# Kernel optimization log

Measured on AMD Instinct MI355X. Metric: run time of the kernel, lower is better.

The kernel has to match this reference:

```python
import jax, jax.numpy as jnp
import numpy as np

HIDDEN = 256
HEADS = 8
HEAD_DIM = HIDDEN // HEADS
N = 4096
EPS = 1e-5


def setup_inputs() -> dict:
    key = jax.random.key(0)
    ks = jax.random.split(key, 16)
    s = HIDDEN ** -0.5
    inp = {
        "A": jax.random.uniform(ks[0], (N, N), dtype=jnp.float32),
        "h": jax.random.normal(ks[1], (N, HIDDEN), dtype=jnp.float32),
        # Linear layers stored torch-style as [out, in]
        "Wq": jax.random.normal(ks[2], (HIDDEN, HIDDEN), jnp.float32) * s,
        "bq": jnp.zeros((HIDDEN,), jnp.float32),
        "Wk": jax.random.normal(ks[3], (HIDDEN, HIDDEN), jnp.float32) * s,
        "bk": jnp.zeros((HIDDEN,), jnp.float32),
        "Wv": jax.random.normal(ks[4], (HIDDEN, HIDDEN), jnp.float32) * s,
        "bv": jnp.zeros((HIDDEN,), jnp.float32),
        "Wo": jax.random.normal(ks[5], (HIDDEN, HIDDEN), jnp.float32) * s,
        "bo": jnp.zeros((HIDDEN,), jnp.float32),
        "W1": jax.random.normal(ks[6], (2 * HIDDEN, HIDDEN), jnp.float32) * s,
        "c1": jnp.zeros((2 * HIDDEN,), jnp.float32),
        "W2": jax.random.normal(ks[7], (HIDDEN, 2 * HIDDEN), jnp.float32) * (2 * HIDDEN) ** -0.5,
        "c2": jnp.zeros((HIDDEN,), jnp.float32),
        "g1": jnp.ones((HIDDEN,), jnp.float32),
        "be1": jnp.zeros((HIDDEN,), jnp.float32),
        "g2": jnp.ones((HIDDEN,), jnp.float32),
        "be2": jnp.zeros((HIDDEN,), jnp.float32),
    }
    return inp


def _batchnorm(x, gamma, beta):
    # BatchNorm1d training mode: biased batch stats over node axis
    mean = x.mean(axis=0)
    var = ((x - mean) ** 2).mean(axis=0)
    return (x - mean) * jax.lax.rsqrt(var + EPS) * gamma + beta


def _mha(A, h, Wq, bq, Wk, bk, Wv, bv, Wo, bo):
    n = h.shape[0]
    scaling = HEAD_DIM ** -0.5
    # NOTE: raw reshape [N, H*d] -> (H, N, d), exactly as the torch code (no transpose)
    q = ((h @ Wq.T + bq).reshape(HEADS, n, HEAD_DIM)) * scaling
    k = (h @ Wk.T + bk).reshape(HEADS, n, HEAD_DIM)
    v = (h @ Wv.T + bv).reshape(HEADS, n, HEAD_DIM)
    t = jnp.einsum('hnd,hmd->hnm', q, k)          # [H, N, N]
    attn = jax.nn.softmax(t * A, axis=2)          # multiplicative adjacency mask
    out = jnp.einsum('hnm,hmd->hnd', attn, v)     # [H, N, d]
    return out.reshape(n, -1) @ Wo.T + bo         # raw reshape back, as in torch


def reference(A, h, Wq, bq, Wk, bk, Wv, bv, Wo, bo, W1, c1, W2, c2, g1, be1, g2, be2):
    h1 = h
    x = _mha(A, h, Wq, bq, Wk, bk, Wv, bv, Wo, bo)
    x = _batchnorm(x + h1, g1, be1)
    h2 = x
    x = jax.nn.relu(x @ W1.T + c1) @ W2.T + c2
    return _batchnorm(h2 + x, g2, be2)
```

## Files before the change

kernel.cpp:

```cpp
#include <hip/hip_runtime.h>

#define N_NODES 4096
#define HID 256
#define NHEADS 8
#define HDIM 32
#define EPSV 1e-5f
#define M2LOG 11.541560327111707f

typedef __bf16 bf16x8 __attribute__((ext_vector_type(8)));
typedef __bf16 bf16x4 __attribute__((ext_vector_type(4)));
typedef float f32x4 __attribute__((ext_vector_type(4)));

__device__ inline float fexp2(float x) {
    float r;
    asm("v_exp_f32 %0, %1" : "=v"(r) : "v"(x));
    return r;
}

__device__ inline uint4 pack8(float4 a, float4 b) {
    bf16x8 p;
    p[0]=(__bf16)a.x; p[1]=(__bf16)a.y; p[2]=(__bf16)a.z; p[3]=(__bf16)a.w;
    p[4]=(__bf16)b.x; p[5]=(__bf16)b.y; p[6]=(__bf16)b.z; p[7]=(__bf16)b.w;
    return __builtin_bit_cast(uint4, p);
}
__device__ inline float4 nmad4(float4 x, float4 s, float4 sh) {
    return make_float4(fmaf(x.x,s.x,sh.x), fmaf(x.y,s.y,sh.y),
                       fmaf(x.z,s.z,sh.z), fmaf(x.w,s.w,sh.w));
}

__launch_bounds__(256)
__global__ void gemm_mfma(const float* __restrict__ X, const float* __restrict__ W,
                          const float* __restrict__ bias, const float* __restrict__ resid,
                          float* __restrict__ C,
                          const float* __restrict__ nscale, const float* __restrict__ nshift,
                          const float* __restrict__ rscale, const float* __restrict__ rshift,
                          int M, int N, int K, float scale, int do_relu) {
    __shared__ uint4 xl[2][512];
    __shared__ uint4 wl[2][512];
    const int bm = blockIdx.x * 64, bn = blockIdx.y * 64;
    const int t = threadIdx.x;
    const int w = t >> 6, l = t & 63, g = l >> 4, nl = l & 15;
    const int srow = t >> 3, seg = t & 7;
    const int sx = (seg & 3) << 1;
    const int d0 = seg*64 + (srow ^ sx);
    const int d1 = seg*64 + ((srow + 32) ^ sx);
    const float* xp = X + (size_t)(bm + srow)*K + seg*8;
    const float* wp = W + (size_t)(bn + srow)*K + seg*8;
    const size_t rstep = (size_t)32*K;

    f32x4 acc[4];
    #pragma unroll
    for (int nf = 0; nf < 4; ++nf) acc[nf] = (f32x4){0.f,0.f,0.f,0.f};

    {
        float4 x0 = *(const float4*)(xp),          x1 = *(const float4*)(xp + 4);
        float4 x2 = *(const float4*)(xp + rstep),  x3 = *(const float4*)(xp + rstep + 4);
        if (nscale) {
            float4 s0 = *(const float4*)(nscale + seg*8), s1 = *(const float4*)(nscale + seg*8 + 4);
            float4 h0 = *(const float4*)(nshift + seg*8), h1 = *(const float4*)(nshift + seg*8 + 4);
            x0 = nmad4(x0,s0,h0); x1 = nmad4(x1,s1,h1);
            x2 = nmad4(x2,s0,h0); x3 = nmad4(x3,s1,h1);
        }
        float4 w0 = *(const float4*)(wp),          w1 = *(const float4*)(wp + 4);
        float4 w2 = *(const float4*)(wp + rstep),  w3 = *(const float4*)(wp + rstep + 4);
        xl[0][d0] = pack8(x0, x1); xl[0][d1] = pack8(x2, x3);
        wl[0][d0] = pack8(w0, w1); wl[0][d1] = pack8(w2, w3);
    }
    __syncthreads();

    for (int k0 = 0; k0 < K; k0 += 64) {
        const int cur = (k0 >> 6) & 1;
        const bool nxt = (k0 + 64) < K;
        float4 nx0, nx1, nx2, nx3, nw0, nw1, nw2, nw3;
        if (nxt) {
            const int kk = k0 + 64;
            nx0 = *(const float4*)(xp + kk);          nx1 = *(const float4*)(xp + kk + 4);
            nx2 = *(const float4*)(xp + rstep + kk);  nx3 = *(const float4*)(xp + rstep + kk + 4);
            if (nscale) {
                float4 s0 = *(const float4*)(nscale + kk + seg*8), s1 = *(const float4*)(nscale + kk + seg*8 + 4);
                float4 h0 = *(const float4*)(nshift + kk + seg*8), h1 = *(const float4*)(nshift + kk + seg*8 + 4);
                nx0 = nmad4(nx0,s0,h0); nx1 = nmad4(nx1,s1,h1);
                nx2 = nmad4(nx2,s0,h0); nx3 = nmad4(nx3,s1,h1);
            }
            nw0 = *(const float4*)(wp + kk);          nw1 = *(const float4*)(wp + kk + 4);
            nw2 = *(const float4*)(wp + rstep + kk);  nw3 = *(const float4*)(wp + rstep + kk + 4);
        }
        __builtin_amdgcn_s_setprio(1);
        #pragma unroll
        for (int ks = 0; ks < 2; ++ks) {
            bf16x8 af = __builtin_bit_cast(bf16x8, xl[cur][(ks*4 + g)*64 + ((w*16 + nl) ^ (g << 1))]);
            #pragma unroll
            for (int nf = 0; nf < 4; ++nf) {
                bf16x8 bfr = __builtin_bit_cast(bf16x8, wl[cur][(ks*4 + g)*64 + ((nf*16 + nl) ^ (g << 1))]);
                acc[nf] = __builtin_amdgcn_mfma_f32_16x16x32_bf16(af, bfr, acc[nf], 0, 0, 0);
            }
        }
        __builtin_amdgcn_s_setprio(0);
        if (nxt) {
            xl[cur^1][d0] = pack8(nx0, nx1); xl[cur^1][d1] = pack8(nx2, nx3);
            wl[cur^1][d0] = pack8(nw0, nw1); wl[cur^1][d1] = pack8(nw2, nw3);
        }
        __syncthreads();
    }

    #pragma unroll
    for (int nf = 0; nf < 4; ++nf) {
        const int col = bn + nf*16 + nl;
        const float bb = bias[col];
        float rs = 1.f, rh = 0.f;
        if (rscale) { rs = rscale[col]; rh = rshift[col]; }
        #pragma unroll
        for (int r = 0; r < 4; ++r) {
            const int row = bm + w*16 + g*4 + r;
            float v = acc[nf][r] + bb;
            if (resid) {
                float rv = resid[(size_t)row*N + col];
                v += rscale ? fmaf(rv, rs, rh) : rv;
            }
            v *= scale;
            if (do_relu) v = fmaxf(v, 0.f);
            C[(size_t)row*N + col] = v;
        }
    }
}

__launch_bounds__(256)
__global__ void gemm_qkv(const float* __restrict__ X,
                         const float* __restrict__ Wq, const float* __restrict__ Wk,
                         const float* __restrict__ Wv, const float* __restrict__ bq,
                         const float* __restrict__ bk, const float* __restrict__ bv,
                         __bf16* __restrict__ qhat, __bf16* __restrict__ khat,
                         __bf16* __restrict__ vhat) {
    const int K = 256;
    __shared__ uint4 xl[2][512];
    __shared__ uint4 wl[2][512];
    const int z = blockIdx.z;
    const float* W = (z == 0) ? Wq : (z == 1) ? Wk : Wv;
    const float* bias = (z == 0) ? bq : (z == 1) ? bk : bv;
    __bf16* hat = (z == 0) ? qhat : (z == 1) ? khat : vhat;
    const float scale = (z == 0) ? 0.25506595325f : 1.f;

    const int bm = blockIdx.x * 64, bn = blockIdx.y * 64;
    const int t = threadIdx.x;
    const int w = t >> 6, l = t & 63, g = l >> 4, nl = l & 15;
    const int srow = t >> 3, seg = t & 7;
    const int sx = (seg & 3) << 1;
    const int d0 = seg*64 + (srow ^ sx);
    const int d1 = seg*64 + ((srow + 32) ^ sx);
    const float* xp = X + (size_t)(bm + srow)*K + seg*8;
    const float* wp = W + (size_t)(bn + srow)*K + seg*8;
    const size_t rstep = (size_t)32*K;

    f32x4 acc[4];
    #pragma unroll
    for (int nf = 0; nf < 4; ++nf) acc[nf] = (f32x4){0.f,0.f,0.f,0.f};

    {
        float4 x0 = *(const float4*)(xp),          x1 = *(const float4*)(xp + 4);
        float4 x2 = *(const float4*)(xp + rstep),  x3 = *(const float4*)(xp + rstep + 4);
        float4 w0 = *(const float4*)(wp),          w1 = *(const float4*)(wp + 4);
        float4 w2 = *(const float4*)(wp + rstep),  w3 = *(const float4*)(wp + rstep + 4);
        xl[0][d0] = pack8(x0, x1); xl[0][d1] = pack8(x2, x3);
        wl[0][d0] = pack8(w0, w1); wl[0][d1] = pack8(w2, w3);
    }
    __syncthreads();

    for (int k0 = 0; k0 < K; k0 += 64) {
        const int cur = (k0 >> 6) & 1;
        const bool nxt = (k0 + 64) < K;
        float4 nx0, nx1, nx2, nx3, nw0, nw1, nw2, nw3;
        if (nxt) {
            nx0 = *(const float4*)(xp + k0 + 64);          nx1 = *(const float4*)(xp + k0 + 68);
            nx2 = *(const float4*)(xp + rstep + k0 + 64);  nx3 = *(const float4*)(xp + rstep + k0 + 68);
            nw0 = *(const float4*)(wp + k0 + 64);          nw1 = *(const float4*)(wp + k0 + 68);
            nw2 = *(const float4*)(wp + rstep + k0 + 64);  nw3 = *(const float4*)(wp + rstep + k0 + 68);
        }
        __builtin_amdgcn_s_setprio(1);
        #pragma unroll
        for (int ks = 0; ks < 2; ++ks) {
            bf16x8 af = __builtin_bit_cast(bf16x8, xl[cur][(ks*4 + g)*64 + ((w*16 + nl) ^ (g << 1))]);
            #pragma unroll
            for (int nf = 0; nf < 4; ++nf) {
                bf16x8 bfr = __builtin_bit_cast(bf16x8, wl[cur][(ks*4 + g)*64 + ((nf*16 + nl) ^ (g << 1))]);
                acc[nf] = __builtin_amdgcn_mfma_f32_16x16x32_bf16(af, bfr, acc[nf], 0, 0, 0);
            }
        }
        __builtin_amdgcn_s_setprio(0);
        if (nxt) {
            xl[cur^1][d0] = pack8(nx0, nx1); xl[cur^1][d1] = pack8(nx2, nx3);
            wl[cur^1][d0] = pack8(nw0, nw1); wl[cur^1][d1] = pack8(nw2, nw3);
        }
        __syncthreads();
    }

    #pragma unroll
    for (int nf = 0; nf < 4; ++nf) {
        const int col = bn + nf*16 + nl;
        const float bb = bias[col];
        #pragma unroll
        for (int r = 0; r < 4; ++r) {
            const int row = bm + w*16 + g*4 + r;
            float v = (acc[nf][r] + bb) * scale;
            const int hh = row >> 9;
            const int nn = ((row & 511) << 3) | (col >> 5);
            hat[((size_t)(hh*4096 + nn))*32 + (col & 31)] = (__bf16)v;
        }
    }
}

__launch_bounds__(256)
__global__ void transpose_vhat(const __bf16* __restrict__ vhat, __bf16* __restrict__ vT) {
    const int h = blockIdx.y, n0 = blockIdx.x * 64;
    __shared__ __bf16 tile[64][40];
    const int t = threadIdx.x;
    {
        int n = t >> 2, dd0 = (t & 3) * 8;
        *(uint4*)&tile[n][dd0] = *(const uint4*)(vhat + ((size_t)(h*4096 + n0 + n))*32 + dd0);
    }
    __syncthreads();
    {
        int d = t >> 3, ns = (t & 7) * 8;
        uint4 ov;
        __bf16* op = (__bf16*)&ov;
        #pragma unroll
        for (int j = 0; j < 8; ++j) op[j] = tile[ns + j][d];
        *(uint4*)(vT + ((size_t)(h*32 + d))*4096 + n0 + ns) = ov;
    }
}

__launch_bounds__(256)
__global__ void attn_mfma(const __bf16* __restrict__ qh, const __bf16* __restrict__ kh,
                          const __bf16* __restrict__ vT, const float* __restrict__ A,
                          float* __restrict__ Opart, float* __restrict__ Lpart, int mlen) {
    const int h = blockIdx.y;
    const int n0 = blockIdx.x * 64;
    const int z = blockIdx.z;
    const int m_begin = z * mlen, m_end = m_begin + mlen;
    const int t = threadIdx.x;
    const int w = t >> 6, l = t & 63;
    const int g = l >> 4, nl = l & 15;
    const int nlx = nl ^ (g << 1);
    const int nq = n0 + w*16 + nl;

    __shared__ uint4 k_lds[2][256];
    __shared__ uint4 v_lds[2][256];
    __shared__ uint4 p_lds[4][128];

    bf16x8 qf = *(const bf16x8*)(qh + ((size_t)(h*4096 + nq))*32 + g*8);

    f32x4 oacc[2];
    oacc[0] = (f32x4){0.f,0.f,0.f,0.f};
    oacc[1] = (f32x4){0.f,0.f,0.f,0.f};
    float Li = 0.f;
    const float* Arow = A + (size_t)nq * N_NODES;

    const int km_row = t >> 2, km_dseg = t & 3;
    const __bf16* kbase = kh + ((size_t)h*4096 + km_row)*32 + km_dseg*8;
    const int kdst = (((km_row >> 4)*4 + km_dseg) << 4) | ((km_row & 15) ^ (km_dseg << 1));
    const int vd = t >> 3, vmseg = t & 7;
    const __bf16* vbase = vT + ((size_t)h*32 + vd)*4096 + vmseg*8;
    const int vdst = ((((vd >> 4)*2 + (vmseg >> 2))*4 + (vmseg & 3)) << 4) | ((vd & 15) ^ ((vmseg & 3) << 1));

    {
        k_lds[0][kdst] = *(const uint4*)(kbase + (size_t)m_begin*32);
        v_lds[0][vdst] = *(const uint4*)(vbase + m_begin);
    }
    float4 ar0 = *(const float4*)(Arow + m_begin + 0*16 + g*4);
    float4 ar1 = *(const float4*)(Arow + m_begin + 1*16 + g*4);
    float4 ar2 = *(const float4*)(Arow + m_begin + 2*16 + g*4);
    float4 ar3 = *(const float4*)(Arow + m_begin + 3*16 + g*4);
    __syncthreads();

    for (int m0 = m_begin; m0 < m_end; m0 += 64) {
        const int cur = ((m0 - m_begin) >> 6) & 1;
        const bool nxt = (m0 + 64) < m_end;
        uint4 krN, vrN;
        float4 an0, an1, an2, an3;
        if (nxt) {
            krN = *(const uint4*)(kbase + (size_t)(m0 + 64)*32);
            vrN = *(const uint4*)(vbase + (m0 + 64));
            an0 = *(const float4*)(Arow + m0 + 64 + 0*16 + g*4);
            an1 = *(const float4*)(Arow + m0 + 64 + 1*16 + g*4);
            an2 = *(const float4*)(Arow + m0 + 64 + 2*16 + g*4);
            an3 = *(const float4*)(Arow + m0 + 64 + 3*16 + g*4);
        }

        f32x4 st[4];
        __builtin_amdgcn_s_setprio(1);
        #pragma unroll
        for (int tt = 0; tt < 4; ++tt) {
            bf16x8 kf = __builtin_bit_cast(bf16x8, k_lds[cur][(tt*4 + g)*16 + nlx]);
            f32x4 zz = (f32x4){0.f,0.f,0.f,0.f};
            st[tt] = __builtin_amdgcn_mfma_f32_16x16x32_bf16(kf, qf, zz, 0, 0, 0);
        }
        __builtin_amdgcn_s_setprio(0);

        float p[4][4];
        p[0][0]=fexp2(fmaf(st[0][0],ar0.x,-M2LOG)); p[0][1]=fexp2(fmaf(st[0][1],ar0.y,-M2LOG));
        p[0][2]=fexp2(fmaf(st[0][2],ar0.z,-M2LOG)); p[0][3]=fexp2(fmaf(st[0][3],ar0.w,-M2LOG));
        p[1][0]=fexp2(fmaf(st[1][0],ar1.x,-M2LOG)); p[1][1]=fexp2(fmaf(st[1][1],ar1.y,-M2LOG));
        p[1][2]=fexp2(fmaf(st[1][2],ar1.z,-M2LOG)); p[1][3]=fexp2(fmaf(st[1][3],ar1.w,-M2LOG));
        p[2][0]=fexp2(fmaf(st[2][0],ar2.x,-M2LOG)); p[2][1]=fexp2(fmaf(st[2][1],ar2.y,-M2LOG));
        p[2][2]=fexp2(fmaf(st[2][2],ar2.z,-M2LOG)); p[2][3]=fexp2(fmaf(st[2][3],ar2.w,-M2LOG));
        p[3][0]=fexp2(fmaf(st[3][0],ar3.x,-M2LOG)); p[3][1]=fexp2(fmaf(st[3][1],ar3.y,-M2LOG));
        p[3][2]=fexp2(fmaf(st[3][2],ar3.z,-M2LOG)); p[3][3]=fexp2(fmaf(st[3][3],ar3.w,-M2LOG));

        float sm[4];
        #pragma unroll
        for (int tt = 0; tt < 4; ++tt)
            sm[tt] = (p[tt][0] + p[tt][1]) + (p[tt][2] + p[tt][3]);
        Li += (sm[0] + sm[1]) + (sm[2] + sm[3]);

        #pragma unroll
        for (int tt = 0; tt < 4; ++tt) {
            bf16x4 pk;
            #pragma unroll
            for (int r = 0; r < 4; ++r) pk[r] = (__bf16)p[tt][r];
            const int seg = (tt >> 1)*4 + 2*(tt & 1) + (g >> 1);
            const int uw = seg*16 + (nl ^ ((seg & 3) << 1));
            *(bf16x4*)((char*)&p_lds[w][0] + uw*16 + (g & 1)*8) = pk;
        }

        __builtin_amdgcn_s_setprio(1);
        #pragma unroll
        for (int kt = 0; kt < 2; ++kt) {
            bf16x8 pf = __builtin_bit_cast(bf16x8, p_lds[w][(kt*4 + g)*16 + nlx]);
            #pragma unroll
            for (int dt = 0; dt < 2; ++dt) {
                bf16x8 vf = __builtin_bit_cast(bf16x8, v_lds[cur][((dt*2 + kt)*4 + g)*16 + nlx]);
                oacc[dt] = __builtin_amdgcn_mfma_f32_16x16x32_bf16(vf, pf, oacc[dt], 0, 0, 0);
            }
        }
        __builtin_amdgcn_s_setprio(0);

        if (nxt) {
            k_lds[cur^1][kdst] = krN;
            v_lds[cur^1][vdst] = vrN;
            ar0 = an0; ar1 = an1; ar2 = an2; ar3 = an3;
        }
        __syncthreads();
    }

    float* ob = Opart + (((size_t)(z*NHEADS + h))*4096 + nq)*32;
    *(float4*)(ob + 0*16 + g*4) = make_float4(oacc[0][0], oacc[0][1], oacc[0][2], oacc[0][3]);
    *(float4*)(ob + 1*16 + g*4) = make_float4(oacc[1][0], oacc[1][1], oacc[1][2], oacc[1][3]);
    Li += __shfl_xor(Li, 16);
    Li += __shfl_xor(Li, 32);
    if (g == 0) Lpart[(z*NHEADS + h)*4096 + nq] = Li;
}

__launch_bounds__(256)
__global__ void attn_combine(const float* __restrict__ Opart, const float* __restrict__ Lpart,
                             float* __restrict__ AO, int nsplit) {
    const int idx4 = (blockIdx.x * 256 + threadIdx.x) * 4;
    const int hn = idx4 >> 5;
    float L = 0.f;
    float4 acc = make_float4(0.f, 0.f, 0.f, 0.f);
    for (int zz = 0; zz < nsplit; ++zz) {
        L += Lpart[zz*32768 + hn];
        float4 o = *(const float4*)(Opart + (size_t)zz*1048576 + idx4);
        acc.x += o.x; acc.y += o.y; acc.z += o.z; acc.w += o.w;
    }
    const float inv = 1.f / L;
    *(float4*)(AO + idx4) = make_float4(acc.x*inv, acc.y*inv, acc.z*inv, acc.w*inv);
}

__launch_bounds__(256)
__global__ void colstats_part(const float* __restrict__ X, float* __restrict__ ps,
                              float* __restrict__ pq) {
    const int b = blockIdx.x, t = threadIdx.x;
    float s = 0.f, q = 0.f;
    const float* p = X + (size_t)b*64*HID + t;
    #pragma unroll 8
    for (int r = 0; r < 64; ++r) {
        float v = p[r*HID];
        s += v; q = fmaf(v, v, q);
    }
    ps[b*HID + t] = s;
    pq[b*HID + t] = q;
}

__launch_bounds__(256)
__global__ void colstats_fin(const float* __restrict__ ps, const float* __restrict__ pq,
                             const float* __restrict__ gam, const float* __restrict__ bet,
                             float* __restrict__ scl, float* __restrict__ shf) {
    const int c = threadIdx.x;
    float s = 0.f, q = 0.f;
    #pragma unroll 8
    for (int b = 0; b < 64; ++b) { s += ps[b*HID + c]; q += pq[b*HID + c]; }
    const float m = s * (1.f/4096.f);
    const float rstd = rsqrtf(q*(1.f/4096.f) - m*m + EPSV);
    const float sc = rstd * gam[c];
    scl[c] = sc;
    shf[c] = fmaf(-m, sc, bet[c]);
}

__launch_bounds__(256)
__global__ void bnorm_apply4(const float* __restrict__ X, const float* __restrict__ scl,
                             const float* __restrict__ shf, float* __restrict__ Y) {
    const int base = (blockIdx.x * 256 + threadIdx.x) * 4;
    const int c = base & (HID - 1);
    float4 x = *(const float4*)(X + base);
    float4 o;
    o.x = fmaf(x.x, scl[c+0], shf[c+0]);
    o.y = fmaf(x.y, scl[c+1], shf[c+1]);
    o.z = fmaf(x.z, scl[c+2], shf[c+2]);
    o.w = fmaf(x.w, scl[c+3], shf[c+3]);
    *(float4*)(Y + base) = o;
}

extern "C" void kernel_launch(void* const* d_in, const int* in_sizes, int n_in,
                              void* d_out, int out_size, void* d_ws, size_t ws_size,
                              hipStream_t stream) {
    const float* A  = (const float*)d_in[0];
    const float* h  = (const float*)d_in[1];
    const float* Wq = (const float*)d_in[2];
    const float* bq = (const float*)d_in[3];
    const float* Wk = (const float*)d_in[4];
    const float* bk = (const float*)d_in[5];
    const float* Wv = (const float*)d_in[6];
    const float* bv = (const float*)d_in[7];
    const float* Wo = (const float*)d_in[8];
    const float* bo = (const float*)d_in[9];
    const float* W1 = (const float*)d_in[10];
    const float* c1 = (const float*)d_in[11];
    const float* W2 = (const float*)d_in[12];
    const float* c2 = (const float*)d_in[13];
    const float* g1 = (const float*)d_in[14];
    const float* be1= (const float*)d_in[15];
    const float* g2 = (const float*)d_in[16];
    const float* be2= (const float*)d_in[17];

    char* wsb = (char*)d_ws;
    const size_t MiB = (size_t)1 << 20;
    const int nsplit = (ws_size >= 27*MiB) ? 4 : (ws_size >= 19*MiB) ? 2 : 1;
    const int mlen = N_NODES / nsplit;

    __bf16* qhat = (__bf16*)(wsb + 0*MiB);
    __bf16* khat = (__bf16*)(wsb + 2*MiB);
    __bf16* vhat = (__bf16*)(wsb + 4*MiB);
    __bf16* vT   = (__bf16*)(wsb + 6*MiB);
    float* Opart = (float*)(wsb + 8*MiB);
    float* Lpart = (float*)(wsb + 8*MiB + (size_t)nsplit*4*MiB);
    char* statb  = wsb + 8*MiB + (size_t)nsplit*4*MiB + 1*MiB;
    float* partS = (float*)statb;
    float* partQ = partS + 64*HID;
    float* scale1 = partQ + 64*HID;
    float* shift1 = scale1 + HID;
    float* scale2 = shift1 + HID;
    float* shift2 = scale2 + HID;
    float* AO = (float*)(wsb + 0*MiB);
    float* Y1 = (float*)(wsb + 4*MiB);
    float* F1 = (float*)(wsb + 8*MiB);
    float* Y2 = (float*)(wsb + 0*MiB);

    gemm_qkv<<<dim3(64, 4, 3), 256, 0, stream>>>(h, Wq, Wk, Wv, bq, bk, bv, qhat, khat, vhat);
    transpose_vhat<<<dim3(64, 8), 256, 0, stream>>>(vhat, vT);

    attn_mfma<<<dim3(64, 8, nsplit), 256, 0, stream>>>(qhat, khat, vT, A, Opart, Lpart, mlen);
    attn_combine<<<1024, 256, 0, stream>>>(Opart, Lpart, AO, nsplit);

    gemm_mfma<<<dim3(64, 4), 256, 0, stream>>>(AO, Wo, bo, h, Y1,
                                               nullptr, nullptr, nullptr, nullptr,
                                               4096, 256, 256, 1.f, 0);

    colstats_part<<<64, 256, 0, stream>>>(Y1, partS, partQ);
    colstats_fin<<<1, 256, 0, stream>>>(partS, partQ, g1, be1, scale1, shift1);

    gemm_mfma<<<dim3(64, 8), 256, 0, stream>>>(Y1, W1, c1, nullptr, F1,
                                               scale1, shift1, nullptr, nullptr,
                                               4096, 512, 256, 1.f, 1);
    gemm_mfma<<<dim3(64, 4), 256, 0, stream>>>(F1, W2, c2, Y1, Y2,
                                               nullptr, nullptr, scale1, shift1,
                                               4096, 256, 512, 1.f, 0);

    colstats_part<<<64, 256, 0, stream>>>(Y2, partS, partQ);
    colstats_fin<<<1, 256, 0, stream>>>(partS, partQ, g2, be2, scale2, shift2);
    bnorm_apply4<<<1024, 256, 0, stream>>>(Y2, scale2, shift2, (float*)d_out);
}
```

Baseline: 149.5 us.

## Share A tile across all heads per block and store partial outputs in bf16

The attention kernel now runs one 512-thread block per 64-row query tile with one wave per head. The block stages the fp32 adjacency tile in LDS once and shares it across all 8 heads, where before each head re-read A from global memory. K and V fragments are now read straight from global memory instead of being staged in LDS, and each wave handles four 16-row query subtiles. Partial outputs are stored in bf16 and the split count over the key axis doubles. This trades more register pressure, bf16 rounding of partial sums and uncached K/V reads for an eightfold cut in A traffic.

```diff
diff --git a/kernel.cpp b/kernel.cpp
--- a/kernel.cpp
+++ b/kernel.cpp
@@ -228,129 +228,128 @@
     }
 }
 
-__launch_bounds__(256)
+__launch_bounds__(512, 4)
 __global__ void attn_mfma(const __bf16* __restrict__ qh, const __bf16* __restrict__ kh,
                           const __bf16* __restrict__ vT, const float* __restrict__ A,
-                          float* __restrict__ Opart, float* __restrict__ Lpart, int mlen) {
-    const int h = blockIdx.y;
+                          __bf16* __restrict__ Opart, float* __restrict__ Lpart, int mlen) {
+    __shared__ float A_lds[2][64][68];
+    __shared__ __bf16 p_lds[NHEADS][64][40];
+
+    const int t = threadIdx.x;
+    const int w = t >> 6;
+    const int l = t & 63, g = l >> 4, nl = l & 15;
     const int n0 = blockIdx.x * 64;
-    const int z = blockIdx.z;
-    const int m_begin = z * mlen, m_end = m_begin + mlen;
-    const int t = threadIdx.x;
-    const int w = t >> 6, l = t & 63;
-    const int g = l >> 4, nl = l & 15;
-    const int nlx = nl ^ (g << 1);
-    const int nq = n0 + w*16 + nl;
-
-    __shared__ uint4 k_lds[2][256];
-    __shared__ uint4 v_lds[2][256];
-    __shared__ uint4 p_lds[4][128];
-
-    bf16x8 qf = *(const bf16x8*)(qh + ((size_t)(h*4096 + nq))*32 + g*8);
-
-    f32x4 oacc[2];
-    oacc[0] = (f32x4){0.f,0.f,0.f,0.f};
-    oacc[1] = (f32x4){0.f,0.f,0.f,0.f};
-    float Li = 0.f;
-    const float* Arow = A + (size_t)nq * N_NODES;
-
-    const int km_row = t >> 2, km_dseg = t & 3;
-    const __bf16* kbase = kh + ((size_t)h*4096 + km_row)*32 + km_dseg*8;
-    const int kdst = (((km_row >> 4)*4 + km_dseg) << 4) | ((km_row & 15) ^ (km_dseg << 1));
-    const int vd = t >> 3, vmseg = t & 7;
-    const __bf16* vbase = vT + ((size_t)h*32 + vd)*4096 + vmseg*8;
-    const int vdst = ((((vd >> 4)*2 + (vmseg >> 2))*4 + (vmseg & 3)) << 4) | ((vd & 15) ^ ((vmseg & 3) << 1));
-
+    const int z = blockIdx.y;
+    const int m_begin = z * mlen;
+    const int nsteps = mlen >> 6;
+
+    bf16x8 qf[4];
+    #pragma unroll
+    for (int nt = 0; nt < 4; ++nt)
+        qf[nt] = *(const bf16x8*)(qh + ((size_t)(w*4096 + n0 + nt*16 + nl))*32 + g*8);
+
+    f32x4 oacc[4][2];
+    #pragma unroll
+    for (int nt = 0; nt < 4; ++nt) {
+        oacc[nt][0] = (f32x4){0.f,0.f,0.f,0.f};
+        oacc[nt][1] = (f32x4){0.f,0.f,0.f,0.f};
+    }
+    float Li[4] = {0.f, 0.f, 0.f, 0.f};
+
+    const int aq = t >> 3, am = (t & 7) * 8;
+    const float* Abase = A + (size_t)(n0 + aq)*N_NODES + m_begin + am;
     {
-        k_lds[0][kdst] = *(const uint4*)(kbase + (size_t)m_begin*32);
-        v_lds[0][vdst] = *(const uint4*)(vbase + m_begin);
-    }
-    float4 ar0 = *(const float4*)(Arow + m_begin + 0*16 + g*4);
-    float4 ar1 = *(const float4*)(Arow + m_begin + 1*16 + g*4);
-    float4 ar2 = *(const float4*)(Arow + m_begin + 2*16 + g*4);
-    float4 ar3 = *(const float4*)(Arow + m_begin + 3*16 + g*4);
+        float4 a0 = *(const float4*)(Abase);
+        float4 a1 = *(const float4*)(Abase + 4);
+        *(float4*)&A_lds[0][aq][am] = a0;
+        *(float4*)&A_lds[0][aq][am+4] = a1;
+    }
     __syncthreads();
 
-    for (int m0 = m_begin; m0 < m_end; m0 += 64) {
-        const int cur = ((m0 - m_begin) >> 6) & 1;
-        const bool nxt = (m0 + 64) < m_end;
-        uint4 krN, vrN;
-        float4 an0, an1, an2, an3;
-        if (nxt) {
-            krN = *(const uint4*)(kbase + (size_t)(m0 + 64)*32);
-            vrN = *(const uint4*)(vbase + (m0 + 64));
-            an0 = *(const float4*)(Arow + m0 + 64 + 0*16 + g*4);
-            an1 = *(const float4*)(Arow + m0 + 64 + 1*16 + g*4);
-            an2 = *(const float4*)(Arow + m0 + 64 + 2*16 + g*4);
-            an3 = *(const float4*)(Arow + m0 + 64 + 3*16 + g*4);
-        }
-
-        f32x4 st[4];
-        __builtin_amdgcn_s_setprio(1);
-        #pragma unroll
-        for (int tt = 0; tt < 4; ++tt) {
-            bf16x8 kf = __builtin_bit_cast(bf16x8, k_lds[cur][(tt*4 + g)*16 + nlx]);
-            f32x4 zz = (f32x4){0.f,0.f,0.f,0.f};
-            st[tt] = __builtin_amdgcn_mfma_f32_16x16x32_bf16(kf, qf, zz, 0, 0, 0);
-        }
-        __builtin_amdgcn_s_setprio(0);
-
-        float p[4][4];
-        p[0][0]=fexp2(fmaf(st[0][0],ar0.x,-M2LOG)); p[0][1]=fexp2(fmaf(st[0][1],ar0.y,-M2LOG));
-        p[0][2]=fexp2(fmaf(st[0][2],ar0.z,-M2LOG)); p[0][3]=fexp2(fmaf(st[0][3],ar0.w,-M2LOG));
-        p[1][0]=fexp2(fmaf(st[1][0],ar1.x,-M2LOG)); p[1][1]=fexp2(fmaf(st[1][1],ar1.y,-M2LOG));
-        p[1][2]=fexp2(fmaf(st[1][2],ar1.z,-M2LOG)); p[1][3]=fexp2(fmaf(st[1][3],ar1.w,-M2LOG));
-        p[2][0]=fexp2(fmaf(st[2][0],ar2.x,-M2LOG)); p[2][1]=fexp2(fmaf(st[2][1],ar2.y,-M2LOG));
-        p[2][2]=fexp2(fmaf(st[2][2],ar2.z,-M2LOG)); p[2][3]=fexp2(fmaf(st[2][3],ar2.w,-M2LOG));
-        p[3][0]=fexp2(fmaf(st[3][0],ar3.x,-M2LOG)); p[3][1]=fexp2(fmaf(st[3][1],ar3.y,-M2LOG));
-        p[3][2]=fexp2(fmaf(st[3][2],ar3.z,-M2LOG)); p[3][3]=fexp2(fmaf(st[3][3],ar3.w,-M2LOG));
-
-        float sm[4];
-        #pragma unroll
-        for (int tt = 0; tt < 4; ++tt)
-            sm[tt] = (p[tt][0] + p[tt][1]) + (p[tt][2] + p[tt][3]);
-        Li += (sm[0] + sm[1]) + (sm[2] + sm[3]);
-
-        #pragma unroll
-        for (int tt = 0; tt < 4; ++tt) {
-            bf16x4 pk;
+    const __bf16* kbase = kh + (size_t)w*4096*32;
+    const __bf16* vbase = vT + (size_t)w*32*4096;
+
+    for (int s = 0; s < nsteps; ++s) {
+        const int m0 = m_begin + s*64;
+        const int cur = s & 1;
+        const bool nxt = (s + 1) < nsteps;
+        float4 a0n, a1n;
+        if (nxt) {
+            a0n = *(const float4*)(Abase + (s+1)*64);
+            a1n = *(const float4*)(Abase + (s+1)*64 + 4);
+        }
+
+        #pragma unroll
+        for (int half = 0; half < 2; ++half) {
+            bf16x8 vf[2];
             #pragma unroll
-            for (int r = 0; r < 4; ++r) pk[r] = (__bf16)p[tt][r];
-            const int seg = (tt >> 1)*4 + 2*(tt & 1) + (g >> 1);
-            const int uw = seg*16 + (nl ^ ((seg & 3) << 1));
-            *(bf16x4*)((char*)&p_lds[w][0] + uw*16 + (g & 1)*8) = pk;
-        }
-
-        __builtin_amdgcn_s_setprio(1);
-        #pragma unroll
-        for (int kt = 0; kt < 2; ++kt) {
-            bf16x8 pf = __builtin_bit_cast(bf16x8, p_lds[w][(kt*4 + g)*16 + nlx]);
+            for (int dt = 0; dt < 2; ++dt)
+                vf[dt] = *(const bf16x8*)(vbase + (size_t)(dt*16 + nl)*4096 + m0 + half*32 + g*8);
+
             #pragma unroll
-            for (int dt = 0; dt < 2; ++dt) {
-                bf16x8 vf = __builtin_bit_cast(bf16x8, v_lds[cur][((dt*2 + kt)*4 + g)*16 + nlx]);
-                oacc[dt] = __builtin_amdgcn_mfma_f32_16x16x32_bf16(vf, pf, oacc[dt], 0, 0, 0);
-            }
-        }
-        __builtin_amdgcn_s_setprio(0);
-
-        if (nxt) {
-            k_lds[cur^1][kdst] = krN;
-            v_lds[cur^1][vdst] = vrN;
-            ar0 = an0; ar1 = an1; ar2 = an2; ar3 = an3;
+            for (int ts = 0; ts < 2; ++ts) {
+                const int tt = half*2 + ts;
+                bf16x8 kf = *(const bf16x8*)(kbase + (size_t)(m0 + tt*16 + nl)*32 + g*8);
+                f32x4 st[4];
+                __builtin_amdgcn_s_setprio(1);
+                #pragma unroll
+                for (int nt = 0; nt < 4; ++nt) {
+                    f32x4 zz = (f32x4){0.f,0.f,0.f,0.f};
+                    st[nt] = __builtin_amdgcn_mfma_f32_16x16x32_bf16(kf, qf[nt], zz, 0, 0, 0);
+                }
+                __builtin_amdgcn_s_setprio(0);
+                #pragma unroll
+                for (int nt = 0; nt < 4; ++nt) {
+                    const f32x4 a4 = *(const f32x4*)&A_lds[cur][nt*16 + nl][tt*16 + g*4];
+                    float p0 = fexp2(fmaf(st[nt][0], a4[0], -M2LOG));
+                    float p1 = fexp2(fmaf(st[nt][1], a4[1], -M2LOG));
+                    float p2 = fexp2(fmaf(st[nt][2], a4[2], -M2LOG));
+                    float p3 = fexp2(fmaf(st[nt][3], a4[3], -M2LOG));
+                    Li[nt] += (p0 + p1) + (p2 + p3);
+                    bf16x4 pk;
+                    pk[0] = (__bf16)p0; pk[1] = (__bf16)p1;
+                    pk[2] = (__bf16)p2; pk[3] = (__bf16)p3;
+                    *(bf16x4*)&p_lds[w][nt*16 + nl][ts*16 + g*4] = pk;
+                }
+            }
+
+            __builtin_amdgcn_s_setprio(1);
+            #pragma unroll
+            for (int nt = 0; nt < 4; ++nt) {
+                bf16x8 pf = *(const bf16x8*)&p_lds[w][nt*16 + nl][g*8];
+                #pragma unroll
+                for (int dt = 0; dt < 2; ++dt)
+                    oacc[nt][dt] = __builtin_amdgcn_mfma_f32_16x16x32_bf16(vf[dt], pf, oacc[nt][dt], 0, 0, 0);
+            }
+            __builtin_amdgcn_s_setprio(0);
+        }
+
+        if (nxt) {
+            *(float4*)&A_lds[cur^1][aq][am]   = a0n;
+            *(float4*)&A_lds[cur^1][aq][am+4] = a1n;
         }
         __syncthreads();
     }
 
-    float* ob = Opart + (((size_t)(z*NHEADS + h))*4096 + nq)*32;
-    *(float4*)(ob + 0*16 + g*4) = make_float4(oacc[0][0], oacc[0][1], oacc[0][2], oacc[0][3]);
-    *(float4*)(ob + 1*16 + g*4) = make_float4(oacc[1][0], oacc[1][1], oacc[1][2], oacc[1][3]);
-    Li += __shfl_xor(Li, 16);
-    Li += __shfl_xor(Li, 32);
-    if (g == 0) Lpart[(z*NHEADS + h)*4096 + nq] = Li;
-}
-
-__launch_bounds__(256)
-__global__ void attn_combine(const float* __restrict__ Opart, const float* __restrict__ Lpart,
+    #pragma unroll
+    for (int nt = 0; nt < 4; ++nt) {
+        Li[nt] += __shfl_xor(Li[nt], 16);
+        Li[nt] += __shfl_xor(Li[nt], 32);
+        const size_t obase = ((size_t)((z*NHEADS + w)*4096) + n0 + nt*16 + nl)*32;
+        #pragma unroll
+        for (int dt = 0; dt < 2; ++dt) {
+            bf16x4 ok;
+            ok[0] = (__bf16)oacc[nt][dt][0]; ok[1] = (__bf16)oacc[nt][dt][1];
+            ok[2] = (__bf16)oacc[nt][dt][2]; ok[3] = (__bf16)oacc[nt][dt][3];
+            *(bf16x4*)(Opart + obase + dt*16 + g*4) = ok;
+        }
+        if (g == 0)
+            Lpart[(z*NHEADS + w)*4096 + n0 + nt*16 + nl] = Li[nt];
+    }
+}
+
+__launch_bounds__(256)
+__global__ void attn_combine(const __bf16* __restrict__ Opart, const float* __restrict__ Lpart,
                              float* __restrict__ AO, int nsplit) {
     const int idx4 = (blockIdx.x * 256 + threadIdx.x) * 4;
     const int hn = idx4 >> 5;
@@ -358,8 +357,9 @@
     float4 acc = make_float4(0.f, 0.f, 0.f, 0.f);
     for (int zz = 0; zz < nsplit; ++zz) {
         L += Lpart[zz*32768 + hn];
-        float4 o = *(const float4*)(Opart + (size_t)zz*1048576 + idx4);
-        acc.x += o.x; acc.y += o.y; acc.z += o.z; acc.w += o.w;
+        bf16x4 o = *(const bf16x4*)(Opart + (size_t)zz*1048576 + idx4);
+        acc.x += (float)o[0]; acc.y += (float)o[1];
+        acc.z += (float)o[2]; acc.w += (float)o[3];
     }
     const float inv = 1.f / L;
     *(float4*)(AO + idx4) = make_float4(acc.x*inv, acc.y*inv, acc.z*inv, acc.w*inv);
@@ -433,16 +433,16 @@
 
     char* wsb = (char*)d_ws;
     const size_t MiB = (size_t)1 << 20;
-    const int nsplit = (ws_size >= 27*MiB) ? 4 : (ws_size >= 19*MiB) ? 2 : 1;
+    const int nsplit = (ws_size >= 26*MiB) ? 8 : (ws_size >= 18*MiB) ? 4 : 2;
     const int mlen = N_NODES / nsplit;
 
     __bf16* qhat = (__bf16*)(wsb + 0*MiB);
     __bf16* khat = (__bf16*)(wsb + 2*MiB);
     __bf16* vhat = (__bf16*)(wsb + 4*MiB);
     __bf16* vT   = (__bf16*)(wsb + 6*MiB);
-    float* Opart = (float*)(wsb + 8*MiB);
-    float* Lpart = (float*)(wsb + 8*MiB + (size_t)nsplit*4*MiB);
-    char* statb  = wsb + 8*MiB + (size_t)nsplit*4*MiB + 1*MiB;
+    __bf16* Opart = (__bf16*)(wsb + 8*MiB);
+    float* Lpart = (float*)(wsb + 8*MiB + (size_t)nsplit*2*MiB);
+    char* statb  = wsb + 8*MiB + (size_t)nsplit*2*MiB + 1*MiB;
     float* partS = (float*)statb;
     float* partQ = partS + 64*HID;
     float* scale1 = partQ + 64*HID;
@@ -457,7 +457,7 @@
     gemm_qkv<<<dim3(64, 4, 3), 256, 0, stream>>>(h, Wq, Wk, Wv, bq, bk, bv, qhat, khat, vhat);
     transpose_vhat<<<dim3(64, 8), 256, 0, stream>>>(vhat, vT);
 
-    attn_mfma<<<dim3(64, 8, nsplit), 256, 0, stream>>>(qhat, khat, vT, A, Opart, Lpart, mlen);
+    attn_mfma<<<dim3(64, nsplit), 512, 0, stream>>>(qhat, khat, vT, A, Opart, Lpart, mlen);
     attn_combine<<<1024, 256, 0, stream>>>(Opart, Lpart, AO, nsplit);
 
     gemm_mfma<<<dim3(64, 4), 256, 0, stream>>>(AO, Wo, bo, h, Y1,
```

New measurement: 166.8 us. 11.5% more time.

## Load K/V fragments straight from global memory and raise split count

Applied to the files above, without the earlier changes.

The attention kernel stops staging K and V tiles in double-buffered shared memory behind block-wide barriers. Each wave now loads its MFMA operand fragments directly from global memory, handles the 64-column step in two 32-column halves with a smaller per-wave P buffer, and never calls __syncthreads. The split-K factor over the key dimension also goes up (up to 8, depending on workspace size), which adds blocks but also more partial output traffic for the combine kernel. The cost is redundant global and L2 reads of K/V across the four waves, and loads that are no longer prefetched a step ahead.

```diff
diff --git a/kernel.cpp b/kernel.cpp
--- a/kernel.cpp
+++ b/kernel.cpp
@@ -232,19 +232,17 @@
 __global__ void attn_mfma(const __bf16* __restrict__ qh, const __bf16* __restrict__ kh,
                           const __bf16* __restrict__ vT, const float* __restrict__ A,
                           float* __restrict__ Opart, float* __restrict__ Lpart, int mlen) {
-    const int h = blockIdx.y;
-    const int n0 = blockIdx.x * 64;
-    const int z = blockIdx.z;
-    const int m_begin = z * mlen, m_end = m_begin + mlen;
+    __shared__ uint4 p_lds[4][64];
     const int t = threadIdx.x;
     const int w = t >> 6, l = t & 63;
     const int g = l >> 4, nl = l & 15;
     const int nlx = nl ^ (g << 1);
+    const int h = blockIdx.y;
+    const int n0 = blockIdx.x * 64;
+    const int z = blockIdx.z;
+    const int m_begin = z * mlen;
+    const int nsteps = mlen >> 6;
     const int nq = n0 + w*16 + nl;
-
-    __shared__ uint4 k_lds[2][256];
-    __shared__ uint4 v_lds[2][256];
-    __shared__ uint4 p_lds[4][128];
 
     bf16x8 qf = *(const bf16x8*)(qh + ((size_t)(h*4096 + nq))*32 + g*8);
 
@@ -252,101 +250,77 @@
     oacc[0] = (f32x4){0.f,0.f,0.f,0.f};
     oacc[1] = (f32x4){0.f,0.f,0.f,0.f};
     float Li = 0.f;
-    const float* Arow = A + (size_t)nq * N_NODES;
-
-    const int km_row = t >> 2, km_dseg = t & 3;
-    const __bf16* kbase = kh + ((size_t)h*4096 + km_row)*32 + km_dseg*8;
-    const int kdst = (((km_row >> 4)*4 + km_dseg) << 4) | ((km_row & 15) ^ (km_dseg << 1));
-    const int vd = t >> 3, vmseg = t & 7;
-    const __bf16* vbase = vT + ((size_t)h*32 + vd)*4096 + vmseg*8;
-    const int vdst = ((((vd >> 4)*2 + (vmseg >> 2))*4 + (vmseg & 3)) << 4) | ((vd & 15) ^ ((vmseg & 3) << 1));
-
-    {
-        k_lds[0][kdst] = *(const uint4*)(kbase + (size_t)m_begin*32);
-        v_lds[0][vdst] = *(const uint4*)(vbase + m_begin);
-    }
-    float4 ar0 = *(const float4*)(Arow + m_begin + 0*16 + g*4);
-    float4 ar1 = *(const float4*)(Arow + m_begin + 1*16 + g*4);
-    float4 ar2 = *(const float4*)(Arow + m_begin + 2*16 + g*4);
-    float4 ar3 = *(const float4*)(Arow + m_begin + 3*16 + g*4);
-    __syncthreads();
-
-    for (int m0 = m_begin; m0 < m_end; m0 += 64) {
-        const int cur = ((m0 - m_begin) >> 6) & 1;
-        const bool nxt = (m0 + 64) < m_end;
-        uint4 krN, vrN;
-        float4 an0, an1, an2, an3;
-        if (nxt) {
-            krN = *(const uint4*)(kbase + (size_t)(m0 + 64)*32);
-            vrN = *(const uint4*)(vbase + (m0 + 64));
-            an0 = *(const float4*)(Arow + m0 + 64 + 0*16 + g*4);
-            an1 = *(const float4*)(Arow + m0 + 64 + 1*16 + g*4);
-            an2 = *(const float4*)(Arow + m0 + 64 + 2*16 + g*4);
-            an3 = *(const float4*)(Arow + m0 + 64 + 3*16 + g*4);
-        }
-
-        f32x4 st[4];
-        __builtin_amdgcn_s_setprio(1);
-        #pragma unroll
-        for (int tt = 0; tt < 4; ++tt) {
-            bf16x8 kf = __builtin_bit_cast(bf16x8, k_lds[cur][(tt*4 + g)*16 + nlx]);
-            f32x4 zz = (f32x4){0.f,0.f,0.f,0.f};
-            st[tt] = __builtin_amdgcn_mfma_f32_16x16x32_bf16(kf, qf, zz, 0, 0, 0);
-        }
-        __builtin_amdgcn_s_setprio(0);
-
-        float p[4][4];
-        p[0][0]=fexp2(fmaf(st[0][0],ar0.x,-M2LOG)); p[0][1]=fexp2(fmaf(st[0][1],ar0.y,-M2LOG));
-        p[0][2]=fexp2(fmaf(st[0][2],ar0.z,-M2LOG)); p[0][3]=fexp2(fmaf(st[0][3],ar0.w,-M2LOG));
-        p[1][0]=fexp2(fmaf(st[1][0],ar1.x,-M2LOG)); p[1][1]=fexp2(fmaf(st[1][1],ar1.y,-M2LOG));
-        p[1][2]=fexp2(fmaf(st[1][2],ar1.z,-M2LOG)); p[1][3]=fexp2(fmaf(st[1][3],ar1.w,-M2LOG));
-        p[2][0]=fexp2(fmaf(st[2][0],ar2.x,-M2LOG)); p[2][1]=fexp2(fmaf(st[2][1],ar2.y,-M2LOG));
-        p[2][2]=fexp2(fmaf(st[2][2],ar2.z,-M2LOG)); p[2][3]=fexp2(fmaf(st[2][3],ar2.w,-M2LOG));
-        p[3][0]=fexp2(fmaf(st[3][0],ar3.x,-M2LOG)); p[3][1]=fexp2(fmaf(st[3][1],ar3.y,-M2LOG));
-        p[3][2]=fexp2(fmaf(st[3][2],ar3.z,-M2LOG)); p[3][3]=fexp2(fmaf(st[3][3],ar3.w,-M2LOG));
-
-        float sm[4];
-        #pragma unroll
-        for (int tt = 0; tt < 4; ++tt)
-            sm[tt] = (p[tt][0] + p[tt][1]) + (p[tt][2] + p[tt][3]);
-        Li += (sm[0] + sm[1]) + (sm[2] + sm[3]);
-
-        #pragma unroll
-        for (int tt = 0; tt < 4; ++tt) {
-            bf16x4 pk;
+
+    const float* Arow = A + (size_t)nq * N_NODES + m_begin;
+    const __bf16* kbase = kh + ((size_t)h*4096 + nl)*32 + g*8;
+    const __bf16* vbase = vT + ((size_t)h*32 + nl)*4096 + g*8;
+
+    float4 ar[4];
+    #pragma unroll
+    for (int tt = 0; tt < 4; ++tt)
+        ar[tt] = *(const float4*)(Arow + tt*16 + g*4);
+
+    for (int s = 0; s < nsteps; ++s) {
+        const int m0 = m_begin + s*64;
+        const bool nxt = (s + 1) < nsteps;
+        float4 arN[4];
+        if (nxt) {
             #pragma unroll
-            for (int r = 0; r < 4; ++r) pk[r] = (__bf16)p[tt][r];
-            const int seg = (tt >> 1)*4 + 2*(tt & 1) + (g >> 1);
-            const int uw = seg*16 + (nl ^ ((seg & 3) << 1));
-            *(bf16x4*)((char*)&p_lds[w][0] + uw*16 + (g & 1)*8) = pk;
-        }
-
-        __builtin_amdgcn_s_setprio(1);
-        #pragma unroll
-        for (int kt = 0; kt < 2; ++kt) {
-            bf16x8 pf = __builtin_bit_cast(bf16x8, p_lds[w][(kt*4 + g)*16 + nlx]);
+            for (int tt = 0; tt < 4; ++tt)
+                arN[tt] = *(const float4*)(Arow + (s+1)*64 + tt*16 + g*4);
+        }
+
+        #pragma unroll
+        for (int half = 0; half < 2; ++half) {
+            const int mh = m0 + half*32;
+            bf16x8 kf0 = *(const bf16x8*)(kbase + (size_t)mh*32);
+            bf16x8 kf1 = *(const bf16x8*)(kbase + (size_t)(mh + 16)*32);
+            bf16x8 vf0 = *(const bf16x8*)(vbase + mh);
+            bf16x8 vf1 = *(const bf16x8*)(vbase + (size_t)16*4096 + mh);
+
             #pragma unroll
-            for (int dt = 0; dt < 2; ++dt) {
-                bf16x8 vf = __builtin_bit_cast(bf16x8, v_lds[cur][((dt*2 + kt)*4 + g)*16 + nlx]);
-                oacc[dt] = __builtin_amdgcn_mfma_f32_16x16x32_bf16(vf, pf, oacc[dt], 0, 0, 0);
+            for (int tt2 = 0; tt2 < 2; ++tt2) {
+                bf16x8 kf = tt2 ? kf1 : kf0;
+                f32x4 zz = (f32x4){0.f,0.f,0.f,0.f};
+                __builtin_amdgcn_s_setprio(1);
+                f32x4 st = __builtin_amdgcn_mfma_f32_16x16x32_bf16(kf, qf, zz, 0, 0, 0);
+                __builtin_amdgcn_s_setprio(0);
+                const float4 a4 = ar[half*2 + tt2];
+                float p0 = fexp2(fmaf(st[0], a4.x, -M2LOG));
+                float p1 = fexp2(fmaf(st[1], a4.y, -M2LOG));
+                float p2 = fexp2(fmaf(st[2], a4.z, -M2LOG));
+                float p3 = fexp2(fmaf(st[3], a4.w, -M2LOG));
+                Li += (p0 + p1) + (p2 + p3);
+                bf16x4 pk;
+                pk[0] = (__bf16)p0; pk[1] = (__bf16)p1;
+                pk[2] = (__bf16)p2; pk[3] = (__bf16)p3;
+                const int seg = tt2*2 + (g >> 1);
+                const int uw = seg*16 + (nl ^ (seg << 1));
+                *(bf16x4*)((char*)&p_lds[w][0] + uw*16 + (g & 1)*8) = pk;
             }
-        }
-        __builtin_amdgcn_s_setprio(0);
-
-        if (nxt) {
-            k_lds[cur^1][kdst] = krN;
-            v_lds[cur^1][vdst] = vrN;
-            ar0 = an0; ar1 = an1; ar2 = an2; ar3 = an3;
-        }
-        __syncthreads();
-    }
-
-    float* ob = Opart + (((size_t)(z*NHEADS + h))*4096 + nq)*32;
-    *(float4*)(ob + 0*16 + g*4) = make_float4(oacc[0][0], oacc[0][1], oacc[0][2], oacc[0][3]);
-    *(float4*)(ob + 1*16 + g*4) = make_float4(oacc[1][0], oacc[1][1], oacc[1][2], oacc[1][3]);
+
+            bf16x8 pf = __builtin_bit_cast(bf16x8, p_lds[w][g*16 + nlx]);
+            __builtin_amdgcn_s_setprio(1);
+            oacc[0] = __builtin_amdgcn_mfma_f32_16x16x32_bf16(vf0, pf, oacc[0], 0, 0, 0);
+            oacc[1] = __builtin_amdgcn_mfma_f32_16x16x32_bf16(vf1, pf, oacc[1], 0, 0, 0);
+            __builtin_amdgcn_s_setprio(0);
+        }
+
+        if (nxt) {
+            #pragma unroll
+            for (int tt = 0; tt < 4; ++tt) ar[tt] = arN[tt];
+        }
+    }
+
     Li += __shfl_xor(Li, 16);
     Li += __shfl_xor(Li, 32);
-    if (g == 0) Lpart[(z*NHEADS + h)*4096 + nq] = Li;
+    float* ob = Opart + ((size_t)(z*NHEADS + h)*4096 + nq)*32;
+    #pragma unroll
+    for (int dt = 0; dt < 2; ++dt)
+        *(float4*)(ob + dt*16 + g*4) = make_float4(oacc[dt][0], oacc[dt][1],
+                                                   oacc[dt][2], oacc[dt][3]);
+    if (g == 0)
+        Lpart[(z*NHEADS + h)*4096 + nq] = Li;
 }
 
 __launch_bounds__(256)
@@ -433,7 +407,7 @@
 
     char* wsb = (char*)d_ws;
     const size_t MiB = (size_t)1 << 20;
-    const int nsplit = (ws_size >= 27*MiB) ? 4 : (ws_size >= 19*MiB) ? 2 : 1;
+    const int nsplit = (ws_size >= 43*MiB) ? 8 : (ws_size >= 26*MiB) ? 4 : 2;
     const int mlen = N_NODES / nsplit;
 
     __bf16* qhat = (__bf16*)(wsb + 0*MiB);
@@ -457,7 +431,7 @@
     gemm_qkv<<<dim3(64, 4, 3), 256, 0, stream>>>(h, Wq, Wk, Wv, bq, bk, bv, qhat, khat, vhat);
     transpose_vhat<<<dim3(64, 8), 256, 0, stream>>>(vhat, vT);
 
-    attn_mfma<<<dim3(64, 8, nsplit), 256, 0, stream>>>(qhat, khat, vT, A, Opart, Lpart, mlen);
+    attn_mfma<<<dim3(64, NHEADS, nsplit), 256, 0, stream>>>(qhat, khat, vT, A, Opart, Lpart, mlen);
     attn_combine<<<1024, 256, 0, stream>>>(Opart, Lpart, AO, nsplit);
 
     gemm_mfma<<<dim3(64, 4), 256, 0, stream>>>(AO, Wo, bo, h, Y1,
```

After: 222.3 us. +48.6%, slower.
